# Kernel tuning notes

Measured on AMD Instinct MI355X. Metric: run time of the kernel, lower is better.

Reference implementation:

```python
import jax, jax.numpy as jnp
import numpy as np

M, F_IN, F_OUT, K = 8192, 32, 32, 5


def setup_inputs() -> dict:
    key = jax.random.key(0)
    k1, k2, k3 = jax.random.split(key, 3)
    x = jax.random.normal(k1, (M, F_IN), dtype=jnp.float32)
    # scale so spectral radius ~O(1); real simplicial Laplacians have bounded spectrum
    L = jax.random.normal(k2, (M, M), dtype=jnp.float32) / jnp.sqrt(jnp.float32(M))
    # xavier-uniform-like scale for W (gain for relu)
    gain = jnp.sqrt(jnp.float32(2.0))
    bound = gain * jnp.sqrt(jnp.float32(6.0 / (F_IN + F_OUT)))
    W = jax.random.uniform(k3, (K, F_IN, F_OUT), dtype=jnp.float32,
                           minval=-bound, maxval=bound)
    return {"x": x, "L": L, "W": W}


def reference(x, L, W):
    """y = sum_{k=0}^{K-1} L^k @ x @ W[k].

    Math identical to the torch module, but computed via the recursive
    propagation z_k = L @ z_{k-1} (z_0 = x), i.e. O(K*M^2*F) instead of
    forming dense matrix powers L^k (O(K*M^3)).
    """
    y0 = x @ W[0]                      # [M, F_out], k = 0 term (L^0 = I)

    def body(z, Wk):
        z = L @ z                      # z_k = L @ z_{k-1}, [M, F_in]
        return z, z @ Wk               # term_k = L^k x W[k], [M, F_out]

    _, terms = jax.lax.scan(body, x, W[1:])   # terms: [K-1, M, F_out]
    return y0 + terms.sum(axis=0)
```

## Files before the change

### kernel.cpp

```cpp
#include <hip/hip_runtime.h>

typedef unsigned short u16;
typedef unsigned int u32;
typedef __bf16 bf16x8 __attribute__((ext_vector_type(8)));
typedef float f32x4 __attribute__((ext_vector_type(4)));
typedef u32 u32x2 __attribute__((ext_vector_type(2)));
typedef u32 u32x4 __attribute__((ext_vector_type(4)));

#define M_DIM 8192
#define S_SPLIT 8
#define CHUNK 1024
#define CROWS 16

__device__ __forceinline__ u16 f2bf(float f) {
  return __builtin_bit_cast(u16, (__bf16)f);
}

union Frag {
  bf16x8 f;
  u16 s[8];
  u32x2 h2[2];
  u32x4 q;
};


__global__ __launch_bounds__(256) void head_kernel(
    const float* __restrict__ x, const float* __restrict__ W0,
    float* __restrict__ y_out, u16* __restrict__ zbt0) {
  __shared__ float Ws[1024];
  __shared__ u16 zsb[256][34];
  const int t = threadIdx.x;
  for (int i = t; i < 1024; i += 256) Ws[i] = W0[i];
  const int m = blockIdx.x * 256 + t;
  float z[32];
  const float4* xr = (const float4*)(x + (size_t)m * 32);
#pragma unroll
  for (int i = 0; i < 8; i++) {
    float4 v = xr[i];
    z[4 * i] = v.x; z[4 * i + 1] = v.y; z[4 * i + 2] = v.z; z[4 * i + 3] = v.w;
  }
#pragma unroll
  for (int c = 0; c < 32; c++) zsb[t][c] = f2bf(z[c]);
  __syncthreads();
  float acc[32];
#pragma unroll
  for (int j = 0; j < 32; j++) acc[j] = 0.f;
#pragma unroll
  for (int c = 0; c < 32; c++) {
#pragma unroll
    for (int j = 0; j < 32; j++) acc[j] += z[c] * Ws[c * 32 + j];
  }
  float4* yo = (float4*)(y_out + (size_t)m * 32);
#pragma unroll
  for (int i = 0; i < 8; i++) {
    float4 v; v.x = acc[4 * i]; v.y = acc[4 * i + 1];
    v.z = acc[4 * i + 2]; v.w = acc[4 * i + 3];
    yo[i] = v;
  }
  const int lane = t & 63, w = t >> 6;
  const int l15 = lane & 15, l4 = lane >> 4;
#pragma unroll
  for (int i = 0; i < 4; i++) {
    int tile = w * 4 + i;
    int ktl = tile >> 1, nt = tile & 1;
    Frag fr;
#pragma unroll
    for (int j = 0; j < 8; j++) fr.s[j] = zsb[ktl * 32 + 8 * l4 + j][nt * 16 + l15];
    size_t kt_g = (size_t)blockIdx.x * 8 + ktl;
    *(u32x4*)(zbt0 + ((kt_g * 2 + nt) * 64 + lane) * 8) = fr.q;
  }
}

__global__ __launch_bounds__(256) void conv_kernel(
    const float* __restrict__ L, const u16* __restrict__ zbt0,
    u16* __restrict__ Lbt, float* __restrict__ z_part) {
  __shared__ u16 At[CROWS][1032];
  __shared__ float red[4][16][33];
  const int t = threadIdx.x;
  const int lane = t & 63, w = t >> 6;
  const int l15 = lane & 15, l4 = lane >> 4;
  const int bx = blockIdx.x;
  const int by = blockIdx.y;
  const int r0 = bx * CROWS;
  const size_t kbase = (size_t)by * CHUNK;

#pragma unroll
  for (int rr = 0; rr < 4; rr++) {
    const int row = w * 4 + rr;
    const float* src = L + (size_t)(r0 + row) * M_DIM + kbase + lane * 4;
#pragma unroll
    for (int seg = 0; seg < 4; seg++) {
      f32x4 v = __builtin_nontemporal_load((const f32x4*)(src + seg * 256));
      u32x2 p;
      p[0] = (u32)f2bf(v[0]) | ((u32)f2bf(v[1]) << 16);
      p[1] = (u32)f2bf(v[2]) | ((u32)f2bf(v[3]) << 16);
      *(u32x2*)&At[row][seg * 256 + lane * 4] = p;
    }
  }
  __syncthreads();

  f32x4 acc0 = {0.f, 0.f, 0.f, 0.f};
  f32x4 acc1 = {0.f, 0.f, 0.f, 0.f};
#pragma unroll
  for (int i = 0; i < 8; i++) {
    const int ktl = w * 8 + i;
    Frag fa;
    fa.q = *(const u32x4*)&At[l15][ktl * 32 + 8 * l4];
    *(u32x4*)(Lbt + ((size_t)(bx * 256 + by * 32 + ktl)) * 512 + lane * 8) = fa.q;
    Frag fb0, fb1;
    size_t bo = ((size_t)((by * 32 + ktl) * 2)) * 512 + lane * 8;
    fb0.q = *(const u32x4*)(zbt0 + bo);
    fb1.q = *(const u32x4*)(zbt0 + bo + 512);
    acc0 = __builtin_amdgcn_mfma_f32_16x16x32_bf16(fa.f, fb0.f, acc0, 0, 0, 0);
    acc1 = __builtin_amdgcn_mfma_f32_16x16x32_bf16(fa.f, fb1.f, acc1, 0, 0, 0);
  }
#pragma unroll
  for (int r = 0; r < 4; r++) {
    red[w][4 * l4 + r][l15] = acc0[r];
    red[w][4 * l4 + r][l15 + 16] = acc1[r];
  }
  __syncthreads();
  const int orow = t >> 4, ocol = t & 15;
  float v0 = red[0][orow][ocol] + red[1][orow][ocol] +
             red[2][orow][ocol] + red[3][orow][ocol];
  float v1 = red[0][orow][ocol + 16] + red[1][orow][ocol + 16] +
             red[2][orow][ocol + 16] + red[3][orow][ocol + 16];
  float* zp = z_part + (size_t)by * (M_DIM * 32) + (size_t)(r0 + orow) * 32;
  zp[ocol] = v0;
  zp[ocol + 16] = v1;
}

__global__ __launch_bounds__(256) void reduce_kernel(
    const float* __restrict__ zp, const float* __restrict__ Wk,
    const float* __restrict__ y_in, float* __restrict__ y_out,
    u16* __restrict__ zbt_out) {
  __shared__ float Ws[1024];
  __shared__ float zs[64][33];
  __shared__ u16 zsb[64][34];
  const int t = threadIdx.x;
  for (int i = t; i < 1024; i += 256) Ws[i] = Wk[i];
  const int ml = t >> 2, cg = t & 3;
  const int m = blockIdx.x * 64 + ml;
  const float* p = zp + (size_t)m * 32 + cg * 8;
  float z8[8];
  {
    float4 lo = *(const float4*)p;
    float4 hi = *(const float4*)(p + 4);
    z8[0] = lo.x; z8[1] = lo.y; z8[2] = lo.z; z8[3] = lo.w;
    z8[4] = hi.x; z8[5] = hi.y; z8[6] = hi.z; z8[7] = hi.w;
  }
#pragma unroll
  for (int s = 1; s < S_SPLIT; s++) {
    const float* ps = p + (size_t)s * (M_DIM * 32);
    float4 lo = *(const float4*)ps;
    float4 hi = *(const float4*)(ps + 4);
    z8[0] += lo.x; z8[1] += lo.y; z8[2] += lo.z; z8[3] += lo.w;
    z8[4] += hi.x; z8[5] += hi.y; z8[6] += hi.z; z8[7] += hi.w;
  }
#pragma unroll
  for (int i = 0; i < 8; i++) {
    zs[ml][cg * 8 + i] = z8[i];
    zsb[ml][cg * 8 + i] = f2bf(z8[i]);
  }
  __syncthreads();
  float acc[8];
  {
    const float4* yi = (const float4*)(y_in + (size_t)m * 32 + cg * 8);
    float4 a0 = yi[0], a1 = yi[1];
    acc[0] = a0.x; acc[1] = a0.y; acc[2] = a0.z; acc[3] = a0.w;
    acc[4] = a1.x; acc[5] = a1.y; acc[6] = a1.z; acc[7] = a1.w;
  }
#pragma unroll
  for (int c = 0; c < 32; c++) {
    float zv = zs[ml][c];
    const float* wr = Ws + c * 32 + cg * 8;
#pragma unroll
    for (int j = 0; j < 8; j++) acc[j] += zv * wr[j];
  }
  float4* yo = (float4*)(y_out + (size_t)m * 32 + cg * 8);
  float4 o0, o1;
  o0.x = acc[0]; o0.y = acc[1]; o0.z = acc[2]; o0.w = acc[3];
  o1.x = acc[4]; o1.y = acc[5]; o1.z = acc[6]; o1.w = acc[7];
  yo[0] = o0; yo[1] = o1;

  const int lane = t & 63, w = t >> 6;
  const int l15 = lane & 15, l4 = lane >> 4;
  const int ktl = w >> 1, nt = w & 1;
  Frag fr;
#pragma unroll
  for (int j = 0; j < 8; j++)
    fr.s[j] = zsb[ktl * 32 + 8 * l4 + j][nt * 16 + l15];
  size_t kt_g = (size_t)blockIdx.x * 2 + ktl;
  *(u32x4*)(zbt_out + ((kt_g * 2 + nt) * 64 + lane) * 8) = fr.q;
}

template <bool LAST>
__global__ __launch_bounds__(512, 4) void fpass_kernel(
    const u16* __restrict__ Lbt, const u16* __restrict__ zbt,
    const float* __restrict__ Wk, const float* __restrict__ y_in,
    float* __restrict__ y_out, u16* __restrict__ zbt_out) {
  __shared__ float red[8][16][33];
  __shared__ float Ws[1024];
  __shared__ float zs[16][33];
  __shared__ u16 zsb[16][36];
  const int t = threadIdx.x;
  const int lane = t & 63, w = t >> 6;
  const int l15 = lane & 15, l4 = lane >> 4;
  const int bx = blockIdx.x;
  for (int i = t; i < 1024; i += 512) Ws[i] = Wk[i];

  const u16* ap = Lbt + ((size_t)bx * 256 + w * 32) * 512 + lane * 8;
  const u16* bp = zbt + (size_t)(w * 32) * 1024 + lane * 8;

  f32x4 acc0 = {0.f, 0.f, 0.f, 0.f};
  f32x4 acc1 = {0.f, 0.f, 0.f, 0.f};
#pragma unroll 8
  for (int kt = 0; kt < 32; kt++) {
    Frag fa, fb0, fb1;
    fa.q = *(const u32x4*)(ap + (size_t)kt * 512);
    fb0.q = *(const u32x4*)(bp + (size_t)kt * 1024);
    fb1.q = *(const u32x4*)(bp + (size_t)kt * 1024 + 512);
    acc0 = __builtin_amdgcn_mfma_f32_16x16x32_bf16(fa.f, fb0.f, acc0, 0, 0, 0);
    acc1 = __builtin_amdgcn_mfma_f32_16x16x32_bf16(fa.f, fb1.f, acc1, 0, 0, 0);
  }
#pragma unroll
  for (int r = 0; r < 4; r++) {
    red[w][4 * l4 + r][l15] = acc0[r];
    red[w][4 * l4 + r][l15 + 16] = acc1[r];
  }
  __syncthreads();
  const int row = t >> 5, j = t & 31;
  float v = 0.f;
#pragma unroll
  for (int s = 0; s < 8; s++) v += red[s][row][j];
  zs[row][j] = v;
  zsb[row][j] = f2bf(v);
  __syncthreads();
  float yv = y_in[(size_t)(bx * 16 + row) * 32 + j];
#pragma unroll
  for (int c = 0; c < 32; c++) yv += zs[row][c] * Ws[c * 32 + j];
  y_out[(size_t)(bx * 16 + row) * 32 + j] = yv;

  if (!LAST && t < 64) {
    const int nt = t >> 5, li = t & 31;
    const int kt = bx >> 1, h = bx & 1;
    Frag fr;
#pragma unroll
    for (int jj = 0; jj < 8; jj++)
      fr.s[jj] = zsb[8 * (li >> 4) + jj][nt * 16 + (li & 15)];
    *(u32x4*)(zbt_out + (size_t)((kt * 2 + nt) * 64 + 32 * h + li) * 8) = fr.q;
  }
}

extern "C" void kernel_launch(void* const* d_in, const int* in_sizes, int n_in,
                              void* d_out, int out_size, void* d_ws,
                              size_t ws_size, hipStream_t stream) {
  const float* x = (const float*)d_in[0];
  const float* L = (const float*)d_in[1];
  const float* W = (const float*)d_in[2];
  float* y = (float*)d_out;
  char* ws = (char*)d_ws;

  const size_t ZT = (size_t)512 << 10;
  u16* zbt0 = (u16*)(ws + 0 * ZT);
  u16* zbt1 = (u16*)(ws + 1 * ZT);
  u16* zbt2 = (u16*)(ws + 2 * ZT);
  u16* zbt3 = (u16*)(ws + 3 * ZT);
  float* z_part = (float*)(ws + ((size_t)2 << 20));
  float* y_acc = (float*)(ws + ((size_t)10 << 20));
  u16* Lbt = (u16*)(ws + ((size_t)12 << 20));

  head_kernel<<<32, 256, 0, stream>>>(x, W, y_acc, zbt0);
  conv_kernel<<<dim3(512, S_SPLIT), 256, 0, stream>>>(L, zbt0, Lbt, z_part);
  reduce_kernel<<<128, 256, 0, stream>>>(z_part, W + 1024, y_acc, y_acc, zbt1);
  fpass_kernel<false><<<512, 512, 0, stream>>>(Lbt, zbt1, W + 2048, y_acc, y_acc, zbt2);
  fpass_kernel<false><<<512, 512, 0, stream>>>(Lbt, zbt2, W + 3072, y_acc, y_acc, zbt3);
  fpass_kernel<true><<<512, 512, 0, stream>>>(Lbt, zbt3, W + 4096, y_acc, y, (u16*)0);
}
```

Before: 186.5 us.

## Fuse split-K conv and reduce into one double-buffered full-row conv kernel

The first propagation step now has each block own 16 full rows of L and walk the whole K dimension in 512-wide chunks with double-buffered LDS staging. The partial-sum buffer and the separate reduce kernel go away, and the W1 projection, y accumulation and bf16 z re-tiling are done in the conv epilogue. This drops one launch and the z_part round trip through memory. In exchange there are only 512 blocks, each looping 16 times with a barrier per chunk, where the old grid had 4096 short blocks, so less parallelism is available to hide the HBM streaming of L.

```diff
diff --git a/kernel.cpp b/kernel.cpp
--- a/kernel.cpp
+++ b/kernel.cpp
@@ -8,9 +8,8 @@
 typedef u32 u32x4 __attribute__((ext_vector_type(4)));
 
 #define M_DIM 8192
-#define S_SPLIT 8
-#define CHUNK 1024
-#define CROWS 16
+#define CCH 512
+#define NCH (M_DIM / CCH)
 
 __device__ __forceinline__ u16 f2bf(float f) {
   return __builtin_bit_cast(u16, (__bf16)f);
@@ -71,127 +70,90 @@
   }
 }
 
-__global__ __launch_bounds__(256) void conv_kernel(
+__global__ __launch_bounds__(512, 4) void conv_kernel(
     const float* __restrict__ L, const u16* __restrict__ zbt0,
-    u16* __restrict__ Lbt, float* __restrict__ z_part) {
-  __shared__ u16 At[CROWS][1032];
-  __shared__ float red[4][16][33];
+    const float* __restrict__ W1, const float* __restrict__ y_in,
+    float* __restrict__ y_out, u16* __restrict__ Lbt,
+    u16* __restrict__ zbt_out) {
+  __shared__ u16 At[2][16][520];
+  __shared__ float red[8][16][33];
+  __shared__ float Ws[1024];
+  __shared__ float zs[16][33];
+  __shared__ u16 zsb[16][36];
   const int t = threadIdx.x;
   const int lane = t & 63, w = t >> 6;
   const int l15 = lane & 15, l4 = lane >> 4;
   const int bx = blockIdx.x;
-  const int by = blockIdx.y;
-  const int r0 = bx * CROWS;
-  const size_t kbase = (size_t)by * CHUNK;
-
-#pragma unroll
-  for (int rr = 0; rr < 4; rr++) {
-    const int row = w * 4 + rr;
-    const float* src = L + (size_t)(r0 + row) * M_DIM + kbase + lane * 4;
+  const int r0 = bx * 16;
+  for (int i = t; i < 1024; i += 512) Ws[i] = W1[i];
+
+  const int srow = t >> 5, scg = t & 31;
+  const float* sbase = L + (size_t)(r0 + srow) * M_DIM + scg * 4;
+
+  auto stage = [&](int c, int buf) {
+    const float* src = sbase + c * CCH;
+    u16* dst = &At[buf][srow][scg * 4];
 #pragma unroll
     for (int seg = 0; seg < 4; seg++) {
-      f32x4 v = __builtin_nontemporal_load((const f32x4*)(src + seg * 256));
+      f32x4 v = __builtin_nontemporal_load((const f32x4*)(src + seg * 128));
       u32x2 p;
       p[0] = (u32)f2bf(v[0]) | ((u32)f2bf(v[1]) << 16);
       p[1] = (u32)f2bf(v[2]) | ((u32)f2bf(v[3]) << 16);
-      *(u32x2*)&At[row][seg * 256 + lane * 4] = p;
+      *(u32x2*)(dst + seg * 128) = p;
     }
-  }
-  __syncthreads();
+  };
 
   f32x4 acc0 = {0.f, 0.f, 0.f, 0.f};
   f32x4 acc1 = {0.f, 0.f, 0.f, 0.f};
-#pragma unroll
-  for (int i = 0; i < 8; i++) {
-    const int ktl = w * 8 + i;
-    Frag fa;
-    fa.q = *(const u32x4*)&At[l15][ktl * 32 + 8 * l4];
-    *(u32x4*)(Lbt + ((size_t)(bx * 256 + by * 32 + ktl)) * 512 + lane * 8) = fa.q;
-    Frag fb0, fb1;
-    size_t bo = ((size_t)((by * 32 + ktl) * 2)) * 512 + lane * 8;
-    fb0.q = *(const u32x4*)(zbt0 + bo);
-    fb1.q = *(const u32x4*)(zbt0 + bo + 512);
-    acc0 = __builtin_amdgcn_mfma_f32_16x16x32_bf16(fa.f, fb0.f, acc0, 0, 0, 0);
-    acc1 = __builtin_amdgcn_mfma_f32_16x16x32_bf16(fa.f, fb1.f, acc1, 0, 0, 0);
-  }
+
+  stage(0, 0);
+  int buf = 0;
+  for (int c = 0; c < NCH; c++) {
+    __syncthreads();
+    if (c + 1 < NCH) stage(c + 1, buf ^ 1);
+#pragma unroll
+    for (int i = 0; i < 2; i++) {
+      const int ktl = c * 16 + w * 2 + i;
+      Frag fa;
+      fa.q = *(const u32x4*)&At[buf][l15][(w * 2 + i) * 32 + 8 * l4];
+      *(u32x4*)(Lbt + ((size_t)bx * 256 + ktl) * 512 + lane * 8) = fa.q;
+      Frag fb0, fb1;
+      size_t bo = ((size_t)ktl * 2) * 512 + lane * 8;
+      fb0.q = *(const u32x4*)(zbt0 + bo);
+      fb1.q = *(const u32x4*)(zbt0 + bo + 512);
+      acc0 = __builtin_amdgcn_mfma_f32_16x16x32_bf16(fa.f, fb0.f, acc0, 0, 0, 0);
+      acc1 = __builtin_amdgcn_mfma_f32_16x16x32_bf16(fa.f, fb1.f, acc1, 0, 0, 0);
+    }
+    buf ^= 1;
+  }
+
 #pragma unroll
   for (int r = 0; r < 4; r++) {
     red[w][4 * l4 + r][l15] = acc0[r];
     red[w][4 * l4 + r][l15 + 16] = acc1[r];
   }
   __syncthreads();
-  const int orow = t >> 4, ocol = t & 15;
-  float v0 = red[0][orow][ocol] + red[1][orow][ocol] +
-             red[2][orow][ocol] + red[3][orow][ocol];
-  float v1 = red[0][orow][ocol + 16] + red[1][orow][ocol + 16] +
-             red[2][orow][ocol + 16] + red[3][orow][ocol + 16];
-  float* zp = z_part + (size_t)by * (M_DIM * 32) + (size_t)(r0 + orow) * 32;
-  zp[ocol] = v0;
-  zp[ocol + 16] = v1;
-}
-
-__global__ __launch_bounds__(256) void reduce_kernel(
-    const float* __restrict__ zp, const float* __restrict__ Wk,
-    const float* __restrict__ y_in, float* __restrict__ y_out,
-    u16* __restrict__ zbt_out) {
-  __shared__ float Ws[1024];
-  __shared__ float zs[64][33];
-  __shared__ u16 zsb[64][34];
-  const int t = threadIdx.x;
-  for (int i = t; i < 1024; i += 256) Ws[i] = Wk[i];
-  const int ml = t >> 2, cg = t & 3;
-  const int m = blockIdx.x * 64 + ml;
-  const float* p = zp + (size_t)m * 32 + cg * 8;
-  float z8[8];
-  {
-    float4 lo = *(const float4*)p;
-    float4 hi = *(const float4*)(p + 4);
-    z8[0] = lo.x; z8[1] = lo.y; z8[2] = lo.z; z8[3] = lo.w;
-    z8[4] = hi.x; z8[5] = hi.y; z8[6] = hi.z; z8[7] = hi.w;
-  }
-#pragma unroll
-  for (int s = 1; s < S_SPLIT; s++) {
-    const float* ps = p + (size_t)s * (M_DIM * 32);
-    float4 lo = *(const float4*)ps;
-    float4 hi = *(const float4*)(ps + 4);
-    z8[0] += lo.x; z8[1] += lo.y; z8[2] += lo.z; z8[3] += lo.w;
-    z8[4] += hi.x; z8[5] += hi.y; z8[6] += hi.z; z8[7] += hi.w;
-  }
-#pragma unroll
-  for (int i = 0; i < 8; i++) {
-    zs[ml][cg * 8 + i] = z8[i];
-    zsb[ml][cg * 8 + i] = f2bf(z8[i]);
-  }
-  __syncthreads();
-  float acc[8];
-  {
-    const float4* yi = (const float4*)(y_in + (size_t)m * 32 + cg * 8);
-    float4 a0 = yi[0], a1 = yi[1];
-    acc[0] = a0.x; acc[1] = a0.y; acc[2] = a0.z; acc[3] = a0.w;
-    acc[4] = a1.x; acc[5] = a1.y; acc[6] = a1.z; acc[7] = a1.w;
-  }
-#pragma unroll
-  for (int c = 0; c < 32; c++) {
-    float zv = zs[ml][c];
-    const float* wr = Ws + c * 32 + cg * 8;
-#pragma unroll
-    for (int j = 0; j < 8; j++) acc[j] += zv * wr[j];
-  }
-  float4* yo = (float4*)(y_out + (size_t)m * 32 + cg * 8);
-  float4 o0, o1;
-  o0.x = acc[0]; o0.y = acc[1]; o0.z = acc[2]; o0.w = acc[3];
-  o1.x = acc[4]; o1.y = acc[5]; o1.z = acc[6]; o1.w = acc[7];
-  yo[0] = o0; yo[1] = o1;
-
-  const int lane = t & 63, w = t >> 6;
-  const int l15 = lane & 15, l4 = lane >> 4;
-  const int ktl = w >> 1, nt = w & 1;
-  Frag fr;
-#pragma unroll
-  for (int j = 0; j < 8; j++)
-    fr.s[j] = zsb[ktl * 32 + 8 * l4 + j][nt * 16 + l15];
-  size_t kt_g = (size_t)blockIdx.x * 2 + ktl;
-  *(u32x4*)(zbt_out + ((kt_g * 2 + nt) * 64 + lane) * 8) = fr.q;
+  const int row = t >> 5, j = t & 31;
+  float v = 0.f;
+#pragma unroll
+  for (int s = 0; s < 8; s++) v += red[s][row][j];
+  zs[row][j] = v;
+  zsb[row][j] = f2bf(v);
+  __syncthreads();
+  float yv = y_in[(size_t)(r0 + row) * 32 + j];
+#pragma unroll
+  for (int c = 0; c < 32; c++) yv += zs[row][c] * Ws[c * 32 + j];
+  y_out[(size_t)(r0 + row) * 32 + j] = yv;
+
+  if (t < 64) {
+    const int nt = t >> 5, li = t & 31;
+    const int kt = bx >> 1, h = bx & 1;
+    Frag fr;
+#pragma unroll
+    for (int jj = 0; jj < 8; jj++)
+      fr.s[jj] = zsb[8 * (li >> 4) + jj][nt * 16 + (li & 15)];
+    *(u32x4*)(zbt_out + (size_t)((kt * 2 + nt) * 64 + 32 * h + li) * 8) = fr.q;
+  }
 }
 
 template <bool LAST>
@@ -266,13 +228,11 @@
   u16* zbt1 = (u16*)(ws + 1 * ZT);
   u16* zbt2 = (u16*)(ws + 2 * ZT);
   u16* zbt3 = (u16*)(ws + 3 * ZT);
-  float* z_part = (float*)(ws + ((size_t)2 << 20));
   float* y_acc = (float*)(ws + ((size_t)10 << 20));
   u16* Lbt = (u16*)(ws + ((size_t)12 << 20));
 
   head_kernel<<<32, 256, 0, stream>>>(x, W, y_acc, zbt0);
-  conv_kernel<<<dim3(512, S_SPLIT), 256, 0, stream>>>(L, zbt0, Lbt, z_part);
-  reduce_kernel<<<128, 256, 0, stream>>>(z_part, W + 1024, y_acc, y_acc, zbt1);
+  conv_kernel<<<512, 512, 0, stream>>>(L, zbt0, W + 1024, y_acc, y_acc, Lbt, zbt1);
   fpass_kernel<false><<<512, 512, 0, stream>>>(Lbt, zbt1, W + 2048, y_acc, y_acc, zbt2);
   fpass_kernel<false><<<512, 512, 0, stream>>>(Lbt, zbt2, W + 3072, y_acc, y_acc, zbt3);
   fpass_kernel<true><<<512, 512, 0, stream>>>(Lbt, zbt3, W + 4096, y_acc, y, (u16*)0);
```

Result: faster. 174.5 us (-6.4%).
